# Kernel optimization log

Hardware: AMD Instinct MI355X
Metric: run time of the kernel (lower is better)

Reference implementation:

```python
import jax, jax.numpy as jnp
import numpy as np

N, E, G, H, F_IN = 100_000, 3_200_000, 256, 16, 7
RRELU_SLOPE = (1.0 / 8.0 + 1.0 / 3.0) / 2.0  # eval-mode RReLU uses mean slope


def rrelu(x):
    return jnp.where(x >= 0, x, RRELU_SLOPE * x)


def gcn_conv(x, edge_index, edge_weight, W, b, n_nodes):
    """PyG GCNConv: add self-loops, symmetric norm, gather-matmul-scatter."""
    row, col = edge_index[0], edge_index[1]
    loop = jnp.arange(n_nodes)
    row = jnp.concatenate([row, loop])
    col = jnp.concatenate([col, loop])
    w = jnp.concatenate([edge_weight, jnp.ones((n_nodes,), x.dtype)])
    deg = jax.ops.segment_sum(w, col, num_segments=n_nodes)
    dis = jnp.where(deg > 0, jax.lax.rsqrt(jnp.maximum(deg, 1e-12)), 0.0)
    norm = dis[row] * w * dis[col]            # [E+N]
    h = x @ W                                  # [N, out]
    msg = h[row] * norm[:, None]               # gather + scale
    return jax.ops.segment_sum(msg, col, num_segments=n_nodes) + b


def max_pool_neighbor_x(x, edge_index, n_nodes):
    row, col = edge_index[0], edge_index[1]
    loop = jnp.arange(n_nodes)
    row = jnp.concatenate([row, loop])
    col = jnp.concatenate([col, loop])
    return jax.ops.segment_max(x[row], col, num_segments=n_nodes)


def setup_inputs() -> dict:
    key = jax.random.key(0)
    ks = jax.random.split(key, 12)
    x = jax.random.normal(ks[0], (N, F_IN), jnp.float32)
    edge_index = jax.random.randint(ks[1], (2, E), 0, N)
    edge_weights = jax.random.uniform(ks[2], (E,), jnp.float32)
    batch = (jnp.arange(N) * G) // N  # sorted, every graph non-empty
    s = 0.2
    W1 = jax.random.normal(ks[3], (F_IN, H), jnp.float32) * s
    b1 = jnp.zeros((H,), jnp.float32)
    W2 = jax.random.normal(ks[4], (H, H), jnp.float32) * s
    b2 = jnp.zeros((H,), jnp.float32)
    Wl1 = jax.random.normal(ks[5], (H, H), jnp.float32) * s
    bl1 = jax.random.normal(ks[6], (H,), jnp.float32) * s
    Wl3 = jax.random.normal(ks[7], (H, H), jnp.float32) * s
    bl3 = jax.random.normal(ks[8], (H,), jnp.float32) * s
    Wl4 = jax.random.normal(ks[9], (H, 1), jnp.float32) * s
    bl4 = jax.random.normal(ks[10], (1,), jnp.float32) * s
    return {"x": x, "edge_index": edge_index, "batch": batch,
            "edge_weights": edge_weights, "W1": W1, "b1": b1, "W2": W2,
            "b2": b2, "Wl1": Wl1, "bl1": bl1, "Wl3": Wl3, "bl3": bl3,
            "Wl4": Wl4, "bl4": bl4}


def reference(x, edge_index, batch, edge_weights, W1, b1, W2, b2,
              Wl1, bl1, Wl3, bl3, Wl4, bl4):
    h = gcn_conv(x, edge_index, edge_weights, W1, b1, N)
    h = max_pool_neighbor_x(h, edge_index, N)
    res = h
    h = gcn_conv(h, edge_index, jnp.ones((E,), h.dtype), W2, b2, N)
    h = jax.nn.relu(res + h)
    g = jax.ops.segment_max(h, batch, num_segments=G)  # global_max_pool
    res = g
    g = rrelu(res + (g @ Wl1 + bl1))
    res = g
    g = rrelu(res + (g @ Wl3 + bl3))
    # dropout p=0.5 in eval mode -> identity
    g = rrelu(g @ Wl4 + bl4)
    return g
```

## Files before the change

kernel.cpp:

```cpp
#include <hip/hip_runtime.h>
#include <hip/hip_fp16.h>
#include <math.h>

#define NN 100000
#define NE 3200000
#define NG 256
#define HD 16
#define FIN 7

#define RB 8
#define RSZ 256
#define NBUK 391
#define NBUKP 400
#define FB 512
#define CHUNK 6250
#define CH2 3125
#define SCB 8
#define LMASK 0x1FFFF

#define SEGN 32
#define SEGB 3125
#define NPW 8

#define PSTRIDE_B 10880
#define SCAP PSTRIDE_B

#define S_DEGW 16777216.0f
#define INV_S_DEGW 5.9604644775390625e-8f

static constexpr float SLOPE = 0.22916666666666666f;

__device__ __forceinline__ float rrelu_f(float a) {
    return a >= 0.f ? a : SLOPE * a;
}

__device__ __forceinline__ float h2f(unsigned short us) {
    __half h = *(__half*)&us;
    return __half2float(h);
}

__device__ __forceinline__ unsigned hmax2u(unsigned a, unsigned b) {
    unsigned r;
    asm volatile("v_pk_max_f16 %0, %1, %2" : "=v"(r) : "v"(a), "v"(b));
    return r;
}


__global__ __launch_bounds__(512) void k_hist(
        const int* __restrict__ col, int* __restrict__ hist) {
    __shared__ int bins[NBUK];
    for (int i = threadIdx.x; i < NBUK; i += 512) bins[i] = 0;
    __syncthreads();
    const int2* c2 = (const int2*)(col + blockIdx.x * CHUNK);
    for (int i = threadIdx.x; i < CH2; i += 512) {
        int2 v = c2[i];
        atomicAdd(&bins[v.x >> RB], 1);
        atomicAdd(&bins[v.y >> RB], 1);
    }
    __syncthreads();
    for (int i = threadIdx.x; i < NBUK; i += 512)
        hist[blockIdx.x * NBUKP + i] = bins[i];
}

__global__ __launch_bounds__(512) void k_scan_a(
        const int* __restrict__ hist, int* __restrict__ pre_t,
        int* __restrict__ tot) {
    __shared__ int s[SCB * (FB + 1)];
    int t = threadIdx.x;
    int c0 = blockIdx.x * SCB;
    for (int i = t; i < SCB * FB; i += 512) {
        int j = i >> 3, c = i & 7;
        int cc = c0 + c;
        s[c * (FB + 1) + j] = (cc < NBUK) ? hist[j * NBUKP + cc] : 0;
    }
    __syncthreads();
    int w = t >> 6, l = t & 63;
    int* sb = &s[w * (FB + 1)];
    int base = l * 8;
    int loc[8];
    int run = 0;
#pragma unroll
    for (int k = 0; k < 8; ++k) { loc[k] = run; run += sb[base + k]; }
    int inc = run;
#pragma unroll
    for (int d = 1; d < 64; d <<= 1) {
        int v = __shfl_up(inc, d, 64);
        if (l >= d) inc += v;
    }
    int excl = inc - run;
    int cc = c0 + w;
    if (cc < NBUK) {
#pragma unroll
        for (int k = 0; k < 8; ++k) sb[base + k] = excl + loc[k];
        if (l == 63) tot[cc] = inc;
    }
    __syncthreads();
    for (int i = t; i < SCB * FB; i += 512) {
        int j = i >> 3, c = i & 7;
        int cc2 = c0 + c;
        if (cc2 < NBUK) pre_t[j * NBUKP + cc2] = s[c * (FB + 1) + j];
    }
}

__global__ __launch_bounds__(512) void k_scan_b(
        const int* __restrict__ tot, int* __restrict__ bstart,
        unsigned* __restrict__ gbuf) {
    __shared__ int s[512];
    int t = threadIdx.x;
    for (int i = t; i < NG * HD; i += 512) gbuf[i] = 0u;
    int v = (t < NBUK) ? tot[t] : 0;
    s[t] = v;
    __syncthreads();
    for (int d = 1; d < 512; d <<= 1) {
        int add = (t >= d) ? s[t - d] : 0;
        __syncthreads();
        s[t] += add;
        __syncthreads();
    }
    if (t < NBUK) bstart[t + 1] = s[t];
    if (t == 0) bstart[0] = 0;
}

__global__ __launch_bounds__(512) void k_fill(
        const int* __restrict__ row, const int* __restrict__ col,
        const float* __restrict__ ew,
        const int* __restrict__ pre_t, const int* __restrict__ bstart,
        unsigned* __restrict__ sp, unsigned short* __restrict__ swh) {
    __shared__ int lcnt[NBUK];
    __shared__ int gofs[NBUK];
    __shared__ int part[512];
    __shared__ unsigned ssp[CHUNK];
    __shared__ unsigned short ssw[CHUNK];
    __shared__ unsigned short sbuk[CHUNK];
    int t = threadIdx.x;
    for (int i = t; i < NBUK; i += 512) {
        lcnt[i] = 0;
        gofs[i] = bstart[i] + pre_t[blockIdx.x * NBUKP + i];
    }
    __syncthreads();
    const int2* c2 = (const int2*)(col + blockIdx.x * CHUNK);
    const int2* r2 = (const int2*)(row + blockIdx.x * CHUNK);
    const float2* e2 = (const float2*)(ew + blockIdx.x * CHUNK);
    for (int i = t; i < CH2; i += 512) {
        int2 v = c2[i];
        atomicAdd(&lcnt[v.x >> RB], 1);
        atomicAdd(&lcnt[v.y >> RB], 1);
    }
    __syncthreads();
    int c = (t < NBUK) ? lcnt[t] : 0;
    part[t] = c;
    __syncthreads();
    for (int d = 1; d < 512; d <<= 1) {
        int add = (t >= d) ? part[t - d] : 0;
        __syncthreads();
        part[t] += add;
        __syncthreads();
    }
    if (t < NBUK) {
        int e = part[t] - c;
        gofs[t] -= e;
        lcnt[t] = e;
    }
    __syncthreads();
    for (int i = t; i < CH2; i += 512) {
        int2 cv = c2[i];
        int2 rv = r2[i];
        float2 wv = e2[i];
        {
            int b = cv.x >> RB;
            int s = atomicAdd(&lcnt[b], 1);
            ssp[s] = ((unsigned)(cv.x & (RSZ - 1)) << 17) | (unsigned)rv.x;
            __half hv = __float2half_rn(wv.x);
            ssw[s] = *(unsigned short*)&hv;
            sbuk[s] = (unsigned short)b;
        }
        {
            int b = cv.y >> RB;
            int s = atomicAdd(&lcnt[b], 1);
            ssp[s] = ((unsigned)(cv.y & (RSZ - 1)) << 17) | (unsigned)rv.y;
            __half hv = __float2half_rn(wv.y);
            ssw[s] = *(unsigned short*)&hv;
            sbuk[s] = (unsigned short)b;
        }
    }
    __syncthreads();
    for (int s = t; s < CHUNK; s += 512) {
        int g = s + gofs[sbuk[s]];
        sp[g] = ssp[s];
        swh[g] = ssw[s];
    }
}

__global__ __launch_bounds__(1024) void k_deg(
        const unsigned* __restrict__ sp, const unsigned short* __restrict__ swh,
        const int* __restrict__ bstart,
        const float* __restrict__ x, const float* __restrict__ W1,
        float* __restrict__ dis1, float* __restrict__ dis2,
        int* __restrict__ pstart, int* __restrict__ cnts,
        unsigned* __restrict__ h1h, unsigned* __restrict__ sp2) {
    __shared__ unsigned long long sdeg[RSZ];
    __shared__ float sdis[RSZ];
    __shared__ float sW1[FIN * HD];
    __shared__ int sscan[RSZ];
    __shared__ int lrank[RSZ];
    __shared__ unsigned sstage[SCAP];
    int t = threadIdx.x;
    if (t < FIN * HD) sW1[t] = W1[t];
    if (t < RSZ) sdeg[t] = 0ULL;
    __syncthreads();
    int s0 = bstart[blockIdx.x], s1 = bstart[blockIdx.x + 1];
    int j = s0 + t;
    for (; j + 3072 < s1; j += 4096) {
        unsigned e0 = sp[j], e1 = sp[j + 1024], e2 = sp[j + 2048], e3 = sp[j + 3072];
        float w0 = h2f(swh[j]), w1 = h2f(swh[j + 1024]);
        float w2 = h2f(swh[j + 2048]), w3 = h2f(swh[j + 3072]);
        atomicAdd(&sdeg[e0 >> 17], (1ULL << 32) |
                  (unsigned long long)(unsigned)__float2int_rn(w0 * S_DEGW));
        atomicAdd(&sdeg[e1 >> 17], (1ULL << 32) |
                  (unsigned long long)(unsigned)__float2int_rn(w1 * S_DEGW));
        atomicAdd(&sdeg[e2 >> 17], (1ULL << 32) |
                  (unsigned long long)(unsigned)__float2int_rn(w2 * S_DEGW));
        atomicAdd(&sdeg[e3 >> 17], (1ULL << 32) |
                  (unsigned long long)(unsigned)__float2int_rn(w3 * S_DEGW));
    }
    for (; j < s1; j += 1024) {
        unsigned e = sp[j];
        float w = h2f(swh[j]);
        atomicAdd(&sdeg[e >> 17], (1ULL << 32) |
                  (unsigned long long)(unsigned)__float2int_rn(w * S_DEGW));
    }
    __syncthreads();
    int node0 = blockIdx.x * RSZ;
    int s0p = blockIdx.x * PSTRIDE_B;
    int cnt_t = 0, pc_t = 0;
    if (t < RSZ) {
        cnt_t = (int)(sdeg[t] >> 32);
        pc_t = (cnt_t + 15) & ~15;
        sscan[t] = pc_t;
    }
    __syncthreads();
    for (int d = 1; d < RSZ; d <<= 1) {
        int add = (t < RSZ && t >= d) ? sscan[t - d] : 0;
        __syncthreads();
        if (t < RSZ) sscan[t] += add;
        __syncthreads();
    }
    if (t < RSZ) {
        int excl = sscan[t] - pc_t;
        lrank[t] = excl;
        if (node0 + t < NN) {
            pstart[node0 + t] = s0p + excl;
            cnts[node0 + t] = cnt_t;
            unsigned long long v = sdeg[t];
            float wsum = (float)(unsigned)(v & 0xFFFFFFFFULL) * INV_S_DEGW;
            float d1 = rsqrtf(wsum + 1.f);
            dis1[node0 + t] = d1;
            sdis[t] = d1;
            dis2[node0 + t] = rsqrtf((float)cnt_t + 1.f);
        }
        int pbase = excl + cnt_t;
        unsigned pv = (unsigned)(node0 + t);
        for (int k = cnt_t; k < pc_t; ++k) {
            int pos = pbase + (k - cnt_t);
            if (pos < SCAP) sstage[pos] = pv;
        }
    }
    __syncthreads();
    for (int k = s0 + t; k < s1; k += 1024) {
        unsigned e = sp[k];
        unsigned short wb = swh[k];
        int pos = atomicAdd(&lrank[e >> 17], 1);
        unsigned packed = ((unsigned)(wb & 0x7FFFu) << 17) | (e & LMASK);
        if (pos < SCAP) sstage[pos] = packed;
    }
    __syncthreads();
    int ptot = sscan[RSZ - 1];
    int lim = ptot < SCAP ? ptot : SCAP;
    for (int k = t; k < lim; k += 1024) sp2[s0p + k] = sstage[k];
    for (int i = t; i < RSZ * 8; i += 1024) {
        int ln = i >> 3, p = i & 7;
        int node = node0 + ln;
        if (node < NN) {
            float a0 = 0.f, a1 = 0.f;
#pragma unroll
            for (int k = 0; k < FIN; ++k) {
                float xv = x[node * FIN + k];
                a0 += xv * sW1[k * HD + 2 * p];
                a1 += xv * sW1[k * HD + 2 * p + 1];
            }
            float d = sdis[ln];
            __half2 hh = __floats2half2_rn(a0 * d, a1 * d);
            h1h[node * 8 + p] = *(unsigned*)&hh;
        }
    }
}

__global__ __launch_bounds__(256) void k_conv1(
        const unsigned* __restrict__ sp2, const int* __restrict__ pstart,
        const int* __restrict__ cnts,
        const unsigned* __restrict__ h1h, const float* __restrict__ dis1,
        const float* __restrict__ b1, unsigned* __restrict__ h1outh) {
    int t = threadIdx.x;
    int wu = __builtin_amdgcn_readfirstlane(t >> 6);
    int l = t & 63;
    int e = l >> 2, p = l & 3;
    float4 bb = ((const float4*)b1)[p];
    const uint2* hv = (const uint2*)h1h;
    int nwbase = blockIdx.x * SEGN + wu * NPW;
    for (int nn = 0; nn < NPW; nn += 4) {
        int nb = nwbase + nn;
        int tC[4], jC[4];
        float a0[4], a1[4], a2[4], a3[4];
#pragma unroll
        for (int c = 0; c < 4; ++c) {
            int node = nb + c;
            int pc = pstart[node];
            tC[c] = (cnts[node] + 15) >> 4;
            jC[c] = pc + e;
            a0[c] = 0.f; a1[c] = 0.f; a2[c] = 0.f; a3[c] = 0.f;
        }
        while ((tC[0] | tC[1] | tC[2] | tC[3]) > 0) {
#pragma unroll
            for (int c = 0; c < 4; ++c) if (tC[c] > 0) {
                unsigned v = sp2[jC[c]];
                uint2 g = hv[(v & LMASK) * 4 + p];
                float wv = h2f((unsigned short)(v >> 17));
                float2 f0 = __half22float2(*(__half2*)&g.x);
                float2 f1 = __half22float2(*(__half2*)&g.y);
                a0[c] += f0.x * wv; a1[c] += f0.y * wv;
                a2[c] += f1.x * wv; a3[c] += f1.y * wv;
                jC[c] += 16; --tC[c];
            }
        }
#pragma unroll
        for (int c = 0; c < 4; ++c) {
            int node = nb + c;
#pragma unroll
            for (int d = 4; d < 64; d <<= 1) {
                a0[c] += __shfl_xor(a0[c], d);
                a1[c] += __shfl_xor(a1[c], d);
                a2[c] += __shfl_xor(a2[c], d);
                a3[c] += __shfl_xor(a3[c], d);
            }
            float dd = dis1[node];
            uint2 sh = hv[node * 4 + p];
            float2 s0 = __half22float2(*(__half2*)&sh.x);
            float2 s1 = __half22float2(*(__half2*)&sh.y);
            float r0 = (a0[c] + s0.x) * dd + bb.x;
            float r1 = (a1[c] + s0.y) * dd + bb.y;
            float r2 = (a2[c] + s1.x) * dd + bb.z;
            float r3 = (a3[c] + s1.y) * dd + bb.w;
            if (e == 0) {
                __half2 h01 = __floats2half2_rn(r0, r1);
                __half2 h23 = __floats2half2_rn(r2, r3);
                ((uint2*)h1outh)[node * 4 + p] =
                    make_uint2(*(unsigned*)&h01, *(unsigned*)&h23);
            }
        }
    }
}

__global__ __launch_bounds__(256) void k_pool_h2(
        const unsigned* __restrict__ sp2, const int* __restrict__ pstart,
        const int* __restrict__ cnts,
        const unsigned* __restrict__ h1outh, const float* __restrict__ W2,
        const float* __restrict__ dis2,
        float4* __restrict__ pool4, unsigned* __restrict__ h2sh) {
    int t = threadIdx.x;
    int wu = __builtin_amdgcn_readfirstlane(t >> 6);
    int l = t & 63;
    int e = l >> 2, p = l & 3;
    float w0 = W2[(4 * p + 0) * HD + e], w1 = W2[(4 * p + 1) * HD + e];
    float w2 = W2[(4 * p + 2) * HD + e], w3 = W2[(4 * p + 3) * HD + e];
    const uint2* hv = (const uint2*)h1outh;
    int nwbase = blockIdx.x * SEGN + wu * NPW;
    for (int nn = 0; nn < NPW; nn += 4) {
        int nb = nwbase + nn;
        int tC[4], jC[4];
        unsigned m01[4], m23[4];
#pragma unroll
        for (int c = 0; c < 4; ++c) {
            int node = nb + c;
            int pc = pstart[node];
            tC[c] = (cnts[node] + 15) >> 4;
            jC[c] = pc + e;
            uint2 sh = hv[node * 4 + p];
            m01[c] = sh.x; m23[c] = sh.y;
        }
        while ((tC[0] | tC[1] | tC[2] | tC[3]) > 0) {
#pragma unroll
            for (int c = 0; c < 4; ++c) if (tC[c] > 0) {
                unsigned v = sp2[jC[c]];
                uint2 g = hv[(v & LMASK) * 4 + p];
                m01[c] = hmax2u(m01[c], g.x);
                m23[c] = hmax2u(m23[c], g.y);
                jC[c] += 16; --tC[c];
            }
        }
#pragma unroll
        for (int c = 0; c < 4; ++c) {
            int node = nb + c;
#pragma unroll
            for (int d = 4; d < 64; d <<= 1) {
                m01[c] = hmax2u(m01[c], __shfl_xor(m01[c], d));
                m23[c] = hmax2u(m23[c], __shfl_xor(m23[c], d));
            }
            float2 f0 = __half22float2(*(__half2*)&m01[c]);
            float2 f1 = __half22float2(*(__half2*)&m23[c]);
            if (e == 0)
                pool4[node * 4 + p] = make_float4(f0.x, f0.y, f1.x, f1.y);
            float partial = f0.x * w0 + f0.y * w1 + f1.x * w2 + f1.y * w3;
            partial += __shfl_xor(partial, 1);
            partial += __shfl_xor(partial, 2);
            float other = __shfl_xor(partial, 4);
            float dd = dis2[node];
            if (((e & 1) == 0) && (p == 0)) {
                __half2 hh = __floats2half2_rn(partial * dd, other * dd);
                h2sh[node * 8 + (e >> 1)] = *(unsigned*)&hh;
            }
        }
    }
}

__global__ __launch_bounds__(256) void k_conv2(
        const unsigned* __restrict__ sp2, const int* __restrict__ pstart,
        const int* __restrict__ cnts,
        const unsigned* __restrict__ h2sh, const float* __restrict__ dis2,
        const float4* __restrict__ pool4, const float* __restrict__ b2,
        unsigned* __restrict__ gbuf) {
    __shared__ unsigned sgmax[2 * HD];
    int t = threadIdx.x;
    if (t < 2 * HD) sgmax[t] = 0u;
    __syncthreads();
    int wu = __builtin_amdgcn_readfirstlane(t >> 6);
    int l = t & 63;
    int e = l >> 2, p = l & 3;
    float4 bb = ((const float4*)b2)[p];
    const uint2* hv = (const uint2*)h2sh;
    int nbase = blockIdx.x * SEGN;
    int gbase = (int)(((unsigned long long)nbase * NG) / NN);
    int nwbase = nbase + wu * NPW;
    for (int nn = 0; nn < NPW; nn += 4) {
        int nb = nwbase + nn;
        int tC[4], jC[4], np[4];
        float a0[4], a1[4], a2[4], a3[4];
#pragma unroll
        for (int c = 0; c < 4; ++c) {
            int node = nb + c;
            int pc = pstart[node], cc = cnts[node];
            tC[c] = (cc + 15) >> 4;
            np[c] = (tC[c] << 4) - cc;
            jC[c] = pc + e;
            a0[c] = 0.f; a1[c] = 0.f; a2[c] = 0.f; a3[c] = 0.f;
        }
        while ((tC[0] | tC[1] | tC[2] | tC[3]) > 0) {
#pragma unroll
            for (int c = 0; c < 4; ++c) if (tC[c] > 0) {
                unsigned v = sp2[jC[c]];
                uint2 g = hv[(v & LMASK) * 4 + p];
                float2 f0 = __half22float2(*(__half2*)&g.x);
                float2 f1 = __half22float2(*(__half2*)&g.y);
                a0[c] += f0.x; a1[c] += f0.y;
                a2[c] += f1.x; a3[c] += f1.y;
                jC[c] += 16; --tC[c];
            }
        }
#pragma unroll
        for (int c = 0; c < 4; ++c) {
            int node = nb + c;
#pragma unroll
            for (int d = 4; d < 64; d <<= 1) {
                a0[c] += __shfl_xor(a0[c], d);
                a1[c] += __shfl_xor(a1[c], d);
                a2[c] += __shfl_xor(a2[c], d);
                a3[c] += __shfl_xor(a3[c], d);
            }
            float dd = dis2[node];
            uint2 sh = hv[node * 4 + p];
            float2 s0 = __half22float2(*(__half2*)&sh.x);
            float2 s1 = __half22float2(*(__half2*)&sh.y);
            float4 pl = pool4[node * 4 + p];
            float cs = 1.f - (float)np[c];
            float r0 = fmaxf(pl.x + (a0[c] + cs * s0.x) * dd + bb.x, 0.f);
            float r1 = fmaxf(pl.y + (a1[c] + cs * s0.y) * dd + bb.y, 0.f);
            float r2 = fmaxf(pl.z + (a2[c] + cs * s1.x) * dd + bb.z, 0.f);
            float r3 = fmaxf(pl.w + (a3[c] + cs * s1.y) * dd + bb.w, 0.f);
            if (e == 0) {
                int lg = (int)(((unsigned long long)node * NG) / NN) - gbase;
                unsigned* sg = &sgmax[lg * HD + 4 * p];
                atomicMax(sg + 0, __float_as_uint(r0));
                atomicMax(sg + 1, __float_as_uint(r1));
                atomicMax(sg + 2, __float_as_uint(r2));
                atomicMax(sg + 3, __float_as_uint(r3));
            }
        }
    }
    __syncthreads();
    if (t < 2 * HD) {
        int lg = t >> 4, f = t & 15;
        int gg = gbase + lg;
        unsigned m = sgmax[t];
        if (gg < NG && m > 0u) atomicMax(&gbuf[gg * HD + f], m);
    }
}

__global__ __launch_bounds__(256) void k_mlp(
        const float* __restrict__ gbuf,
        const float* __restrict__ Wl1, const float* __restrict__ bl1,
        const float* __restrict__ Wl3, const float* __restrict__ bl3,
        const float* __restrict__ Wl4, const float* __restrict__ bl4,
        float* __restrict__ out) {
    __shared__ float sW1[256], sW3[256], sW4[16], sb1[16], sb3[16];
    __shared__ float sb4;
    int tid = threadIdx.x;
    sW1[tid] = Wl1[tid];
    sW3[tid] = Wl3[tid];
    if (tid < 16) { sW4[tid] = Wl4[tid]; sb1[tid] = bl1[tid]; sb3[tid] = bl3[tid]; }
    if (tid == 0) sb4 = bl4[0];
    __syncthreads();

    float v[16], t1[16], t2[16];
#pragma unroll
    for (int f = 0; f < 16; ++f) v[f] = gbuf[tid * 16 + f];
#pragma unroll
    for (int f = 0; f < 16; ++f) {
        float a = sb1[f] + v[f];
#pragma unroll
        for (int k = 0; k < 16; ++k) a += v[k] * sW1[k * 16 + f];
        t1[f] = rrelu_f(a);
    }
#pragma unroll
    for (int f = 0; f < 16; ++f) {
        float a = sb3[f] + t1[f];
#pragma unroll
        for (int k = 0; k < 16; ++k) a += t1[k] * sW3[k * 16 + f];
        t2[f] = rrelu_f(a);
    }
    float o = sb4;
#pragma unroll
    for (int k = 0; k < 16; ++k) o += t2[k] * sW4[k];
    out[tid] = rrelu_f(o);
}

extern "C" void kernel_launch(void* const* d_in, const int* in_sizes, int n_in,
                              void* d_out, int out_size, void* d_ws, size_t ws_size,
                              hipStream_t stream) {
    const float* x   = (const float*)d_in[0];
    const int*   ei  = (const int*)  d_in[1];
    const float* ew  = (const float*)d_in[3];
    const float* W1  = (const float*)d_in[4];
    const float* b1  = (const float*)d_in[5];
    const float* W2  = (const float*)d_in[6];
    const float* b2  = (const float*)d_in[7];
    const float* Wl1 = (const float*)d_in[8];
    const float* bl1 = (const float*)d_in[9];
    const float* Wl3 = (const float*)d_in[10];
    const float* bl3 = (const float*)d_in[11];
    const float* Wl4 = (const float*)d_in[12];
    const float* bl4 = (const float*)d_in[13];
    const int* row = ei;
    const int* col = ei + NE;

    float* ws = (float*)d_ws;
    float* pool  = ws;
    float* dead  = pool + NN * HD;
    float* dis1  = dead + NN * HD;
    float* dis2  = dis1 + NN;
    int*   pstart = (int*)(dis2 + NN);
    int*   cnts  = pstart + NN;
    unsigned* gbuf = (unsigned*)(cnts + NN);
    unsigned* h1h    = gbuf   + NG * HD;
    unsigned* h1outh = h1h    + NN * 8;
    unsigned* h2sh   = h1outh + NN * 8;
    unsigned* sp     = h2sh   + NN * 8;
    unsigned short* swh = (unsigned short*)(sp + NE);
    unsigned* sp2    = (unsigned*)(swh + NE);
    int* tot    = (int*)(sp2 + (size_t)NBUK * PSTRIDE_B);
    int* bstart = tot + NBUK;
    int* hist   = (int*)pool;
    int* pre_t  = (int*)dead;

    k_hist     <<<FB, 512, 0, stream>>>(col, hist);
    k_scan_a   <<<(NBUK + SCB - 1) / SCB, 512, 0, stream>>>(hist, pre_t, tot);
    k_scan_b   <<<1, 512, 0, stream>>>(tot, bstart, gbuf);
    k_fill     <<<FB, 512, 0, stream>>>(row, col, ew, pre_t, bstart, sp, swh);
    k_deg      <<<NBUK, 1024, 0, stream>>>(sp, swh, bstart, x, W1,
                                           dis1, dis2, pstart, cnts, h1h, sp2);
    k_conv1    <<<SEGB, 256, 0, stream>>>(sp2, pstart, cnts, h1h, dis1,
                                          b1, h1outh);
    k_pool_h2  <<<SEGB, 256, 0, stream>>>(sp2, pstart, cnts, h1outh, W2, dis2,
                                          (float4*)pool, h2sh);
    k_conv2    <<<SEGB, 256, 0, stream>>>(sp2, pstart, cnts, h2sh, dis2,
                                          (const float4*)pool, b2, gbuf);
    k_mlp      <<<1, 256, 0, stream>>>((const float*)gbuf, Wl1, bl1, Wl3, bl3,
                                       Wl4, bl4, (float*)d_out);
}
```

Baseline: 262.6 us.

## Batch all 8 node gathers per wave with sentinel rows instead of predicated loops

The three gather kernels (conv1, pool/h2, conv2) now process all NPW=8 nodes of a wave together. They issue 8 index loads, then 8 feature gathers per iteration with no branches, which raises memory-level parallelism. Exhausted nodes are pointed at sentinel rows appended to each feature table: a zero row for sums and a -inf row for max. k_scan_b initializes these rows. The change adds register pressure and some redundant loads for nodes with fewer edges, but removes the divergent per-node predication.

```diff
diff --git a/kernel.cpp b/kernel.cpp
--- a/kernel.cpp
+++ b/kernel.cpp
@@ -21,6 +21,10 @@
 #define SEGN 32
 #define SEGB 3125
 #define NPW 8
+
+#define ZROW ((unsigned)NN)
+#define NROW ((unsigned)(NN + 1))
+#define TROWS (NN + 2)
 
 #define PSTRIDE_B 10880
 #define SCAP PSTRIDE_B
@@ -104,10 +108,17 @@
 
 __global__ __launch_bounds__(512) void k_scan_b(
         const int* __restrict__ tot, int* __restrict__ bstart,
-        unsigned* __restrict__ gbuf) {
+        unsigned* __restrict__ gbuf, unsigned* __restrict__ h1h,
+        unsigned* __restrict__ h1outh, unsigned* __restrict__ h2sh) {
     __shared__ int s[512];
     int t = threadIdx.x;
     for (int i = t; i < NG * HD; i += 512) gbuf[i] = 0u;
+    if (t < 48) {
+        int tab = t >> 4, w = t & 15;
+        unsigned* p = (tab == 0) ? h1h : (tab == 1) ? h1outh : h2sh;
+        unsigned val = (w < 8) ? 0u : 0xFC00FC00u;
+        p[(NN + (w >> 3)) * 8 + (w & 7)] = val;
+    }
     int v = (t < NBUK) ? tot[t] : 0;
     s[t] = v;
     __syncthreads();
@@ -306,56 +317,61 @@
     int e = l >> 2, p = l & 3;
     float4 bb = ((const float4*)b1)[p];
     const uint2* hv = (const uint2*)h1h;
-    int nwbase = blockIdx.x * SEGN + wu * NPW;
-    for (int nn = 0; nn < NPW; nn += 4) {
-        int nb = nwbase + nn;
-        int tC[4], jC[4];
-        float a0[4], a1[4], a2[4], a3[4];
-#pragma unroll
-        for (int c = 0; c < 4; ++c) {
-            int node = nb + c;
-            int pc = pstart[node];
-            tC[c] = (cnts[node] + 15) >> 4;
-            jC[c] = pc + e;
-            a0[c] = 0.f; a1[c] = 0.f; a2[c] = 0.f; a3[c] = 0.f;
-        }
-        while ((tC[0] | tC[1] | tC[2] | tC[3]) > 0) {
-#pragma unroll
-            for (int c = 0; c < 4; ++c) if (tC[c] > 0) {
-                unsigned v = sp2[jC[c]];
-                uint2 g = hv[(v & LMASK) * 4 + p];
-                float wv = h2f((unsigned short)(v >> 17));
-                float2 f0 = __half22float2(*(__half2*)&g.x);
-                float2 f1 = __half22float2(*(__half2*)&g.y);
-                a0[c] += f0.x * wv; a1[c] += f0.y * wv;
-                a2[c] += f1.x * wv; a3[c] += f1.y * wv;
-                jC[c] += 16; --tC[c];
-            }
-        }
-#pragma unroll
-        for (int c = 0; c < 4; ++c) {
-            int node = nb + c;
-#pragma unroll
-            for (int d = 4; d < 64; d <<= 1) {
-                a0[c] += __shfl_xor(a0[c], d);
-                a1[c] += __shfl_xor(a1[c], d);
-                a2[c] += __shfl_xor(a2[c], d);
-                a3[c] += __shfl_xor(a3[c], d);
-            }
-            float dd = dis1[node];
-            uint2 sh = hv[node * 4 + p];
-            float2 s0 = __half22float2(*(__half2*)&sh.x);
-            float2 s1 = __half22float2(*(__half2*)&sh.y);
-            float r0 = (a0[c] + s0.x) * dd + bb.x;
-            float r1 = (a1[c] + s0.y) * dd + bb.y;
-            float r2 = (a2[c] + s1.x) * dd + bb.z;
-            float r3 = (a3[c] + s1.y) * dd + bb.w;
-            if (e == 0) {
-                __half2 h01 = __floats2half2_rn(r0, r1);
-                __half2 h23 = __floats2half2_rn(r2, r3);
-                ((uint2*)h1outh)[node * 4 + p] =
-                    make_uint2(*(unsigned*)&h01, *(unsigned*)&h23);
-            }
+    int nb = blockIdx.x * SEGN + wu * NPW;
+    int tr[NPW], jj[NPW];
+    float a0[NPW], a1[NPW], a2[NPW], a3[NPW];
+    int maxt = 0;
+#pragma unroll
+    for (int c = 0; c < NPW; ++c) {
+        int node = nb + c;
+        tr[c] = (cnts[node] + 15) >> 4;
+        jj[c] = pstart[node] + e;
+        maxt = max(maxt, tr[c]);
+        a0[c] = 0.f; a1[c] = 0.f; a2[c] = 0.f; a3[c] = 0.f;
+    }
+    for (int it = 0; it < maxt; ++it) {
+        unsigned v[NPW];
+#pragma unroll
+        for (int c = 0; c < NPW; ++c) v[c] = sp2[jj[c]];
+        uint2 g[NPW];
+#pragma unroll
+        for (int c = 0; c < NPW; ++c) {
+            unsigned r = (it < tr[c]) ? (v[c] & LMASK) : ZROW;
+            g[c] = hv[r * 4 + p];
+        }
+#pragma unroll
+        for (int c = 0; c < NPW; ++c) {
+            float wv = h2f((unsigned short)(v[c] >> 17));
+            float2 f0 = __half22float2(*(__half2*)&g[c].x);
+            float2 f1 = __half22float2(*(__half2*)&g[c].y);
+            a0[c] += f0.x * wv; a1[c] += f0.y * wv;
+            a2[c] += f1.x * wv; a3[c] += f1.y * wv;
+            if (it + 1 < tr[c]) jj[c] += 16;
+        }
+    }
+#pragma unroll
+    for (int c = 0; c < NPW; ++c) {
+        int node = nb + c;
+#pragma unroll
+        for (int d = 4; d < 64; d <<= 1) {
+            a0[c] += __shfl_xor(a0[c], d);
+            a1[c] += __shfl_xor(a1[c], d);
+            a2[c] += __shfl_xor(a2[c], d);
+            a3[c] += __shfl_xor(a3[c], d);
+        }
+        float dd = dis1[node];
+        uint2 sh = hv[node * 4 + p];
+        float2 s0 = __half22float2(*(__half2*)&sh.x);
+        float2 s1 = __half22float2(*(__half2*)&sh.y);
+        float r0 = (a0[c] + s0.x) * dd + bb.x;
+        float r1 = (a1[c] + s0.y) * dd + bb.y;
+        float r2 = (a2[c] + s1.x) * dd + bb.z;
+        float r3 = (a3[c] + s1.y) * dd + bb.w;
+        if (e == 0) {
+            __half2 h01 = __floats2half2_rn(r0, r1);
+            __half2 h23 = __floats2half2_rn(r2, r3);
+            ((uint2*)h1outh)[node * 4 + p] =
+                make_uint2(*(unsigned*)&h01, *(unsigned*)&h23);
         }
     }
 }
@@ -373,51 +389,56 @@
     float w0 = W2[(4 * p + 0) * HD + e], w1 = W2[(4 * p + 1) * HD + e];
     float w2 = W2[(4 * p + 2) * HD + e], w3 = W2[(4 * p + 3) * HD + e];
     const uint2* hv = (const uint2*)h1outh;
-    int nwbase = blockIdx.x * SEGN + wu * NPW;
-    for (int nn = 0; nn < NPW; nn += 4) {
-        int nb = nwbase + nn;
-        int tC[4], jC[4];
-        unsigned m01[4], m23[4];
-#pragma unroll
-        for (int c = 0; c < 4; ++c) {
-            int node = nb + c;
-            int pc = pstart[node];
-            tC[c] = (cnts[node] + 15) >> 4;
-            jC[c] = pc + e;
-            uint2 sh = hv[node * 4 + p];
-            m01[c] = sh.x; m23[c] = sh.y;
-        }
-        while ((tC[0] | tC[1] | tC[2] | tC[3]) > 0) {
-#pragma unroll
-            for (int c = 0; c < 4; ++c) if (tC[c] > 0) {
-                unsigned v = sp2[jC[c]];
-                uint2 g = hv[(v & LMASK) * 4 + p];
-                m01[c] = hmax2u(m01[c], g.x);
-                m23[c] = hmax2u(m23[c], g.y);
-                jC[c] += 16; --tC[c];
-            }
-        }
-#pragma unroll
-        for (int c = 0; c < 4; ++c) {
-            int node = nb + c;
-#pragma unroll
-            for (int d = 4; d < 64; d <<= 1) {
-                m01[c] = hmax2u(m01[c], __shfl_xor(m01[c], d));
-                m23[c] = hmax2u(m23[c], __shfl_xor(m23[c], d));
-            }
-            float2 f0 = __half22float2(*(__half2*)&m01[c]);
-            float2 f1 = __half22float2(*(__half2*)&m23[c]);
-            if (e == 0)
-                pool4[node * 4 + p] = make_float4(f0.x, f0.y, f1.x, f1.y);
-            float partial = f0.x * w0 + f0.y * w1 + f1.x * w2 + f1.y * w3;
-            partial += __shfl_xor(partial, 1);
-            partial += __shfl_xor(partial, 2);
-            float other = __shfl_xor(partial, 4);
-            float dd = dis2[node];
-            if (((e & 1) == 0) && (p == 0)) {
-                __half2 hh = __floats2half2_rn(partial * dd, other * dd);
-                h2sh[node * 8 + (e >> 1)] = *(unsigned*)&hh;
-            }
+    int nb = blockIdx.x * SEGN + wu * NPW;
+    int tr[NPW], jj[NPW];
+    unsigned m01[NPW], m23[NPW];
+    int maxt = 0;
+#pragma unroll
+    for (int c = 0; c < NPW; ++c) {
+        int node = nb + c;
+        tr[c] = (cnts[node] + 15) >> 4;
+        jj[c] = pstart[node] + e;
+        maxt = max(maxt, tr[c]);
+        uint2 sh = hv[node * 4 + p];
+        m01[c] = sh.x; m23[c] = sh.y;
+    }
+    for (int it = 0; it < maxt; ++it) {
+        unsigned v[NPW];
+#pragma unroll
+        for (int c = 0; c < NPW; ++c) v[c] = sp2[jj[c]];
+        uint2 g[NPW];
+#pragma unroll
+        for (int c = 0; c < NPW; ++c) {
+            unsigned r = (it < tr[c]) ? (v[c] & LMASK) : NROW;
+            g[c] = hv[r * 4 + p];
+        }
+#pragma unroll
+        for (int c = 0; c < NPW; ++c) {
+            m01[c] = hmax2u(m01[c], g[c].x);
+            m23[c] = hmax2u(m23[c], g[c].y);
+            if (it + 1 < tr[c]) jj[c] += 16;
+        }
+    }
+#pragma unroll
+    for (int c = 0; c < NPW; ++c) {
+        int node = nb + c;
+#pragma unroll
+        for (int d = 4; d < 64; d <<= 1) {
+            m01[c] = hmax2u(m01[c], __shfl_xor(m01[c], d));
+            m23[c] = hmax2u(m23[c], __shfl_xor(m23[c], d));
+        }
+        float2 f0 = __half22float2(*(__half2*)&m01[c]);
+        float2 f1 = __half22float2(*(__half2*)&m23[c]);
+        if (e == 0)
+            pool4[node * 4 + p] = make_float4(f0.x, f0.y, f1.x, f1.y);
+        float partial = f0.x * w0 + f0.y * w1 + f1.x * w2 + f1.y * w3;
+        partial += __shfl_xor(partial, 1);
+        partial += __shfl_xor(partial, 2);
+        float other = __shfl_xor(partial, 4);
+        float dd = dis2[node];
+        if (((e & 1) == 0) && (p == 0)) {
+            __half2 hh = __floats2half2_rn(partial * dd, other * dd);
+            h2sh[node * 8 + (e >> 1)] = *(unsigned*)&hh;
         }
     }
 }
@@ -439,60 +460,66 @@
     const uint2* hv = (const uint2*)h2sh;
     int nbase = blockIdx.x * SEGN;
     int gbase = (int)(((unsigned long long)nbase * NG) / NN);
-    int nwbase = nbase + wu * NPW;
-    for (int nn = 0; nn < NPW; nn += 4) {
-        int nb = nwbase + nn;
-        int tC[4], jC[4], np[4];
-        float a0[4], a1[4], a2[4], a3[4];
-#pragma unroll
-        for (int c = 0; c < 4; ++c) {
-            int node = nb + c;
-            int pc = pstart[node], cc = cnts[node];
-            tC[c] = (cc + 15) >> 4;
-            np[c] = (tC[c] << 4) - cc;
-            jC[c] = pc + e;
-            a0[c] = 0.f; a1[c] = 0.f; a2[c] = 0.f; a3[c] = 0.f;
-        }
-        while ((tC[0] | tC[1] | tC[2] | tC[3]) > 0) {
-#pragma unroll
-            for (int c = 0; c < 4; ++c) if (tC[c] > 0) {
-                unsigned v = sp2[jC[c]];
-                uint2 g = hv[(v & LMASK) * 4 + p];
-                float2 f0 = __half22float2(*(__half2*)&g.x);
-                float2 f1 = __half22float2(*(__half2*)&g.y);
-                a0[c] += f0.x; a1[c] += f0.y;
-                a2[c] += f1.x; a3[c] += f1.y;
-                jC[c] += 16; --tC[c];
-            }
-        }
-#pragma unroll
-        for (int c = 0; c < 4; ++c) {
-            int node = nb + c;
-#pragma unroll
-            for (int d = 4; d < 64; d <<= 1) {
-                a0[c] += __shfl_xor(a0[c], d);
-                a1[c] += __shfl_xor(a1[c], d);
-                a2[c] += __shfl_xor(a2[c], d);
-                a3[c] += __shfl_xor(a3[c], d);
-            }
-            float dd = dis2[node];
-            uint2 sh = hv[node * 4 + p];
-            float2 s0 = __half22float2(*(__half2*)&sh.x);
-            float2 s1 = __half22float2(*(__half2*)&sh.y);
-            float4 pl = pool4[node * 4 + p];
-            float cs = 1.f - (float)np[c];
-            float r0 = fmaxf(pl.x + (a0[c] + cs * s0.x) * dd + bb.x, 0.f);
-            float r1 = fmaxf(pl.y + (a1[c] + cs * s0.y) * dd + bb.y, 0.f);
-            float r2 = fmaxf(pl.z + (a2[c] + cs * s1.x) * dd + bb.z, 0.f);
-            float r3 = fmaxf(pl.w + (a3[c] + cs * s1.y) * dd + bb.w, 0.f);
-            if (e == 0) {
-                int lg = (int)(((unsigned long long)node * NG) / NN) - gbase;
-                unsigned* sg = &sgmax[lg * HD + 4 * p];
-                atomicMax(sg + 0, __float_as_uint(r0));
-                atomicMax(sg + 1, __float_as_uint(r1));
-                atomicMax(sg + 2, __float_as_uint(r2));
-                atomicMax(sg + 3, __float_as_uint(r3));
-            }
+    int nb = nbase + wu * NPW;
+    int tr[NPW], jj[NPW], np[NPW];
+    float a0[NPW], a1[NPW], a2[NPW], a3[NPW];
+    int maxt = 0;
+#pragma unroll
+    for (int c = 0; c < NPW; ++c) {
+        int node = nb + c;
+        int cc = cnts[node];
+        tr[c] = (cc + 15) >> 4;
+        np[c] = (tr[c] << 4) - cc;
+        jj[c] = pstart[node] + e;
+        maxt = max(maxt, tr[c]);
+        a0[c] = 0.f; a1[c] = 0.f; a2[c] = 0.f; a3[c] = 0.f;
+    }
+    for (int it = 0; it < maxt; ++it) {
+        unsigned v[NPW];
+#pragma unroll
+        for (int c = 0; c < NPW; ++c) v[c] = sp2[jj[c]];
+        uint2 g[NPW];
+#pragma unroll
+        for (int c = 0; c < NPW; ++c) {
+            unsigned r = (it < tr[c]) ? (v[c] & LMASK) : ZROW;
+            g[c] = hv[r * 4 + p];
+        }
+#pragma unroll
+        for (int c = 0; c < NPW; ++c) {
+            float2 f0 = __half22float2(*(__half2*)&g[c].x);
+            float2 f1 = __half22float2(*(__half2*)&g[c].y);
+            a0[c] += f0.x; a1[c] += f0.y;
+            a2[c] += f1.x; a3[c] += f1.y;
+            if (it + 1 < tr[c]) jj[c] += 16;
+        }
+    }
+#pragma unroll
+    for (int c = 0; c < NPW; ++c) {
+        int node = nb + c;
+#pragma unroll
+        for (int d = 4; d < 64; d <<= 1) {
+            a0[c] += __shfl_xor(a0[c], d);
+            a1[c] += __shfl_xor(a1[c], d);
+            a2[c] += __shfl_xor(a2[c], d);
+            a3[c] += __shfl_xor(a3[c], d);
+        }
+        float dd = dis2[node];
+        uint2 sh = hv[node * 4 + p];
+        float2 s0 = __half22float2(*(__half2*)&sh.x);
+        float2 s1 = __half22float2(*(__half2*)&sh.y);
+        float4 pl = pool4[node * 4 + p];
+        float cs = 1.f - (float)np[c];
+        float r0 = fmaxf(pl.x + (a0[c] + cs * s0.x) * dd + bb.x, 0.f);
+        float r1 = fmaxf(pl.y + (a1[c] + cs * s0.y) * dd + bb.y, 0.f);
+        float r2 = fmaxf(pl.z + (a2[c] + cs * s1.x) * dd + bb.z, 0.f);
+        float r3 = fmaxf(pl.w + (a3[c] + cs * s1.y) * dd + bb.w, 0.f);
+        if (e == 0) {
+            int lg = (int)(((unsigned long long)node * NG) / NN) - gbase;
+            unsigned* sg = &sgmax[lg * HD + 4 * p];
+            atomicMax(sg + 0, __float_as_uint(r0));
+            atomicMax(sg + 1, __float_as_uint(r1));
+            atomicMax(sg + 2, __float_as_uint(r2));
+            atomicMax(sg + 3, __float_as_uint(r3));
         }
     }
     __syncthreads();
@@ -570,9 +597,9 @@
     int*   cnts  = pstart + NN;
     unsigned* gbuf = (unsigned*)(cnts + NN);
     unsigned* h1h    = gbuf   + NG * HD;
-    unsigned* h1outh = h1h    + NN * 8;
-    unsigned* h2sh   = h1outh + NN * 8;
-    unsigned* sp     = h2sh   + NN * 8;
+    unsigned* h1outh = h1h    + TROWS * 8;
+    unsigned* h2sh   = h1outh + TROWS * 8;
+    unsigned* sp     = h2sh   + TROWS * 8;
     unsigned short* swh = (unsigned short*)(sp + NE);
     unsigned* sp2    = (unsigned*)(swh + NE);
     int* tot    = (int*)(sp2 + (size_t)NBUK * PSTRIDE_B);
@@ -582,7 +609,7 @@
 
     k_hist     <<<FB, 512, 0, stream>>>(col, hist);
     k_scan_a   <<<(NBUK + SCB - 1) / SCB, 512, 0, stream>>>(hist, pre_t, tot);
-    k_scan_b   <<<1, 512, 0, stream>>>(tot, bstart, gbuf);
+    k_scan_b   <<<1, 512, 0, stream>>>(tot, bstart, gbuf, h1h, h1outh, h2sh);
     k_fill     <<<FB, 512, 0, stream>>>(row, col, ew, pre_t, bstart, sp, swh);
     k_deg      <<<NBUK, 1024, 0, stream>>>(sp, swh, bstart, x, W1,
                                            dis1, dis2, pstart, cnts, h1h, sp2);
```

After: 242.2 us. 1.08x faster.
